# Kernel optimization log

Measured on AMD Instinct MI355X. Metric: run time of the kernel, lower is better.

The kernel has to match this reference:

```python
import jax, jax.numpy as jnp
import numpy as np

N = 50000      # nodes
E = 800000     # edges (avg degree 16)
F_IN = 512
HID = 128
OUT = 40


def setup_inputs() -> dict:
    key = jax.random.key(0)
    ks = jax.random.split(key, 6)
    x = jax.random.normal(ks[0], (N, F_IN), dtype=jnp.float32)
    edge_index = jax.random.randint(ks[1], (2, E), 0, N, dtype=jnp.int64)
    edge_weight = jax.random.uniform(ks[2], (E,), dtype=jnp.float32)
    # Glorot-ish init for the two GCNConv weight matrices
    W1 = jax.random.normal(ks[3], (F_IN, HID), dtype=jnp.float32) * (1.0 / np.sqrt(F_IN))
    b1 = jnp.zeros((HID,), dtype=jnp.float32)
    W2 = jax.random.normal(ks[4], (HID, OUT), dtype=jnp.float32) * (1.0 / np.sqrt(HID))
    b2 = jnp.zeros((OUT,), dtype=jnp.float32)
    return {"x": x, "edge_index": edge_index, "edge_weight": edge_weight,
            "W1": W1, "b1": b1, "W2": W2, "b2": b2}


def gcn_layer(x, edge_index, edge_weight, W, b):
    """PyG GCNConv (normalize=True, add_self_loops=True):
    out = D^{-1/2} (A + I) D^{-1/2} (x @ W) + b, with weighted edges."""
    n = x.shape[0]
    h = x @ W  # [n, F_out] dense transform before aggregation
    sl = jnp.arange(n)
    row = jnp.concatenate([edge_index[0], sl])   # source nodes
    col = jnp.concatenate([edge_index[1], sl])   # target nodes
    w = jnp.concatenate([edge_weight, jnp.ones((n,), x.dtype)])  # self-loop weight 1
    deg = jax.ops.segment_sum(w, col, num_segments=n)            # in-degree (weighted)
    dinv = jnp.where(deg > 0, jax.lax.rsqrt(deg), 0.0)
    norm = dinv[row] * w * dinv[col]                             # per-edge coefficient
    # gather-source, scale, scatter-add into target
    out = jax.ops.segment_sum(h[row] * norm[:, None], col, num_segments=n)
    return out + b


def reference(x, edge_index, edge_weight, W1, b1, W2, b2):
    h = jax.nn.relu(gcn_layer(x, edge_index, edge_weight, W1, b1))
    # dropout is identity at inference (training=False)
    h = gcn_layer(h, edge_index, edge_weight, W2, b2)
    return jax.nn.log_softmax(h, axis=1)
```

## Files before the change

kernel.cpp:

```cpp
#include <hip/hip_runtime.h>
#include <math.h>

#define N_NODES 50000
#define F_IN    512
#define HID     128
#define OUT_C   40
#define NPAD    48
#define E_EDGES 800000
#define SCAN_BLOCKS 196
#define LDA 40
#define LDK 136
#define MAXDEG 96
#define G1B 391
#define DEGB 3125

typedef __attribute__((ext_vector_type(8))) short short8;
typedef __attribute__((ext_vector_type(4))) float f32x4;

__device__ __forceinline__ unsigned short f2bf(float f) {
    union { float f; unsigned u; } v; v.f = f;
    unsigned u = v.u + 0x7fffu + ((v.u >> 16) & 1u);
    return (unsigned short)(u >> 16);
}
__device__ __forceinline__ float bf2f(unsigned short h) {
    return __uint_as_float((unsigned)h << 16);
}


__global__ void k_init(unsigned long long* __restrict__ packed) {
    int i = blockIdx.x * blockDim.x + threadIdx.x;
    if (i < N_NODES) packed[i] = 0ULL;
}


__global__ __launch_bounds__(256) void k_wprep(const float* __restrict__ W1,
                                               const float* __restrict__ W2,
                                               unsigned short* __restrict__ W1bt,
                                               unsigned short* __restrict__ W2bt) {
    int idx = blockIdx.x * 256 + threadIdx.x;
    if (idx < F_IN * HID) {
        int k = idx & 511, n = idx >> 9;
        W1bt[(size_t)n * F_IN + k] = f2bf(W1[(size_t)k * HID + n]);
    } else if (idx < F_IN * HID + NPAD * HID) {
        int i2 = idx - F_IN * HID;
        int k = i2 & 127, n = i2 >> 7;
        W2bt[n * HID + k] = (n < OUT_C) ? f2bf(W2[(size_t)k * OUT_C + n]) : 0;
    }
}


__global__ __launch_bounds__(256) void k_g1deg(const float* __restrict__ X,
                                               const unsigned short* __restrict__ W1bt,
                                               unsigned short* __restrict__ Hb,
                                               const int* __restrict__ col,
                                               const float* __restrict__ ew,
                                               unsigned long long* __restrict__ packed,
                                               int* __restrict__ rank) {
    const int tid = threadIdx.x;
    if (blockIdx.x >= G1B) {
        int e = (blockIdx.x - G1B) * 256 + tid;
        if (e < E_EDGES) {
            int c = col[e];
            unsigned long long fx = (unsigned long long)(ew[e] * 4294967296.0f);
            unsigned long long old = atomicAdd(&packed[c], (1ULL << 40) | fx);
            rank[e] = (int)(old >> 40);
        }
        return;
    }

    __shared__ __align__(16) unsigned short As[128 * LDA];
    __shared__ __align__(16) unsigned short Bs[128 * LDA];
    const int row0 = blockIdx.x * 128;
    const int lane = tid & 63;
    const int w    = tid >> 6;
    const int quad = lane >> 4;
    const int l16  = lane & 15;
    const int wm   = (w >> 1) * 64;
    const int wn   = (w & 1) * 64;

    f32x4 acc[4][4] = {};

    const int sr = tid >> 1;
    const int kg = (tid & 1) * 16;
    int arow = row0 + sr;
    if (arow >= N_NODES) arow = N_NODES - 1;
    const float*          xp = X + (size_t)arow * F_IN + kg;
    const unsigned short* bp = W1bt + (size_t)sr * F_IN + kg;
    unsigned short* asw = &As[sr * LDA + kg];
    unsigned short* bsw = &Bs[sr * LDA + kg];

    for (int k0 = 0; k0 < F_IN; k0 += 32) {
        float4 xa = *(const float4*)(xp + k0);
        float4 xb = *(const float4*)(xp + k0 + 4);
        float4 xc = *(const float4*)(xp + k0 + 8);
        float4 xd = *(const float4*)(xp + k0 + 12);
        short8 pa, pb;
        pa[0] = (short)f2bf(xa.x); pa[1] = (short)f2bf(xa.y);
        pa[2] = (short)f2bf(xa.z); pa[3] = (short)f2bf(xa.w);
        pa[4] = (short)f2bf(xb.x); pa[5] = (short)f2bf(xb.y);
        pa[6] = (short)f2bf(xb.z); pa[7] = (short)f2bf(xb.w);
        pb[0] = (short)f2bf(xc.x); pb[1] = (short)f2bf(xc.y);
        pb[2] = (short)f2bf(xc.z); pb[3] = (short)f2bf(xc.w);
        pb[4] = (short)f2bf(xd.x); pb[5] = (short)f2bf(xd.y);
        pb[6] = (short)f2bf(xd.z); pb[7] = (short)f2bf(xd.w);
        short8 wa = *(const short8*)(bp + k0);
        short8 wb = *(const short8*)(bp + k0 + 8);

        *(short8*)(asw)     = pa;
        *(short8*)(asw + 8) = pb;
        *(short8*)(bsw)     = wa;
        *(short8*)(bsw + 8) = wb;
        __syncthreads();

        short8 af[4], bf[4];
#pragma unroll
        for (int i = 0; i < 4; i++)
            af[i] = *(const short8*)&As[(wm + i * 16 + l16) * LDA + quad * 8];
#pragma unroll
        for (int j = 0; j < 4; j++)
            bf[j] = *(const short8*)&Bs[(wn + j * 16 + l16) * LDA + quad * 8];
#pragma unroll
        for (int i = 0; i < 4; i++)
#pragma unroll
            for (int j = 0; j < 4; j++)
                acc[i][j] = __builtin_amdgcn_mfma_f32_16x16x32_bf16(
                    af[i], bf[j], acc[i][j], 0, 0, 0);
        __syncthreads();
    }

#pragma unroll
    for (int i = 0; i < 4; i++) {
#pragma unroll
        for (int r = 0; r < 4; r++) {
            int grow = row0 + wm + i * 16 + quad * 4 + r;
            if (grow < N_NODES) {
#pragma unroll
                for (int j = 0; j < 4; j++) {
                    int gcol = wn + j * 16 + l16;
                    Hb[(size_t)grow * HID + gcol] = f2bf(acc[i][j][r]);
                }
            }
        }
    }
}


__global__ __launch_bounds__(256) void k_scan1(const unsigned long long* __restrict__ packed,
                                               int* __restrict__ excl,
                                               int* __restrict__ bsum,
                                               float* __restrict__ dinv) {
    __shared__ int s[256];
    int tid = threadIdx.x;
    int i = blockIdx.x * 256 + tid;
    unsigned long long pk = (i < N_NODES) ? packed[i] : 0ULL;
    int v = (int)(pk >> 40);
    if (i < N_NODES) {
        float d = 1.0f + (float)(pk & 0xFFFFFFFFFFULL) * (1.0f / 4294967296.0f);
        dinv[i] = rsqrtf(d);
    }
    s[tid] = v;
    __syncthreads();
#pragma unroll
    for (int off = 1; off < 256; off <<= 1) {
        int t = (tid >= off) ? s[tid - off] : 0;
        __syncthreads();
        s[tid] += t;
        __syncthreads();
    }
    if (i < N_NODES) excl[i] = s[tid] - v;
    if (tid == 255) bsum[blockIdx.x] = s[255];
}

__global__ __launch_bounds__(256) void k_scan2(int* __restrict__ bsum) {
    __shared__ int s[256];
    int tid = threadIdx.x;
    int v = (tid < SCAN_BLOCKS) ? bsum[tid] : 0;
    s[tid] = v;
    __syncthreads();
#pragma unroll
    for (int off = 1; off < 256; off <<= 1) {
        int t = (tid >= off) ? s[tid - off] : 0;
        __syncthreads();
        s[tid] += t;
        __syncthreads();
    }
    if (tid < SCAN_BLOCKS) bsum[tid] = s[tid] - v;
}

__global__ __launch_bounds__(256) void k_scan3(int* __restrict__ rowptr,
                                               const int* __restrict__ bsum) {
    int i = blockIdx.x * 256 + threadIdx.x;
    if (i < N_NODES) rowptr[i] += bsum[blockIdx.x];
    if (i == 0) rowptr[N_NODES] = E_EDGES;
}


__global__ void k_scatter(const int* __restrict__ row, const int* __restrict__ col,
                          const float* __restrict__ w, const float* __restrict__ dinv,
                          const int* __restrict__ rowptr, const int* __restrict__ rank,
                          int2* __restrict__ es) {
    int e = blockIdx.x * blockDim.x + threadIdx.x;
    if (e < E_EDGES) {
        int r = row[e], c = col[e];
        float pre = dinv[r] * w[e];
        int pos = rowptr[c] + rank[e];
        es[pos] = make_int2(r, __float_as_int(pre));
    }
}


__global__ __launch_bounds__(256) void k_agg1_csr(const int* __restrict__ rowptr,
                                                  const int2* __restrict__ es,
                                                  const float* __restrict__ dinv,
                                                  const unsigned short* __restrict__ H1b,
                                                  const float* __restrict__ b1,
                                                  unsigned short* __restrict__ A1b) {
    __shared__ int2 sE[4][MAXDEG];
    const int tid  = threadIdx.x;
    const int wv   = tid >> 6;
    const int lane = tid & 63;
    const int node = blockIdx.x * 4 + wv;
    if (node >= N_NODES) return;

    const int beg = rowptr[node];
    const int d   = rowptr[node + 1] - beg;
    const int dl  = (d < MAXDEG) ? d : MAXDEG;
    const int dp  = (dl + 7) & ~7;
    for (int p = lane; p < dp; p += 64)
        sE[wv][p] = (p < dl) ? es[beg + p] : make_int2(0, 0);

    const float di = dinv[node];
    const unsigned self = *(const unsigned*)&H1b[(size_t)node * HID + lane * 2];
    float al0 = di * __uint_as_float(self << 16);
    float ah0 = di * __uint_as_float(self & 0xffff0000u);
    float al1 = 0.0f, ah1 = 0.0f, al2 = 0.0f, ah2 = 0.0f, al3 = 0.0f, ah3 = 0.0f;

    for (int p = 0; p < dp; p += 8) {
        int s[8]; float n[8]; unsigned g[8];
#pragma unroll
        for (int j = 0; j < 8; j++) {
            int2 t = sE[wv][p + j];
            s[j] = t.x; n[j] = __int_as_float(t.y);
        }
#pragma unroll
        for (int j = 0; j < 8; j++)
            g[j] = *(const unsigned*)&H1b[(size_t)s[j] * HID + lane * 2];
        al0 = fmaf(__uint_as_float(g[0] << 16), n[0], al0);
        ah0 = fmaf(__uint_as_float(g[0] & 0xffff0000u), n[0], ah0);
        al1 = fmaf(__uint_as_float(g[1] << 16), n[1], al1);
        ah1 = fmaf(__uint_as_float(g[1] & 0xffff0000u), n[1], ah1);
        al2 = fmaf(__uint_as_float(g[2] << 16), n[2], al2);
        ah2 = fmaf(__uint_as_float(g[2] & 0xffff0000u), n[2], ah2);
        al3 = fmaf(__uint_as_float(g[3] << 16), n[3], al3);
        ah3 = fmaf(__uint_as_float(g[3] & 0xffff0000u), n[3], ah3);
        al0 = fmaf(__uint_as_float(g[4] << 16), n[4], al0);
        ah0 = fmaf(__uint_as_float(g[4] & 0xffff0000u), n[4], ah0);
        al1 = fmaf(__uint_as_float(g[5] << 16), n[5], al1);
        ah1 = fmaf(__uint_as_float(g[5] & 0xffff0000u), n[5], ah1);
        al2 = fmaf(__uint_as_float(g[6] << 16), n[6], al2);
        ah2 = fmaf(__uint_as_float(g[6] & 0xffff0000u), n[6], ah2);
        al3 = fmaf(__uint_as_float(g[7] << 16), n[7], al3);
        ah3 = fmaf(__uint_as_float(g[7] & 0xffff0000u), n[7], ah3);
    }
    for (int q = dl; q < d; ++q) {
        int2 t = es[beg + q];
        unsigned g = *(const unsigned*)&H1b[(size_t)t.x * HID + lane * 2];
        float nm = __int_as_float(t.y);
        al0 = fmaf(__uint_as_float(g << 16), nm, al0);
        ah0 = fmaf(__uint_as_float(g & 0xffff0000u), nm, ah0);
    }

    const float accl = (al0 + al1) + (al2 + al3);
    const float acch = (ah0 + ah1) + (ah2 + ah3);
    const int c = lane * 2;
    float rx = fmaxf(fmaf(di, accl, b1[c]), 0.0f);
    float ry = fmaxf(fmaf(di, acch, b1[c + 1]), 0.0f);
    unsigned pack = (unsigned)f2bf(rx) | ((unsigned)f2bf(ry) << 16);
    *(unsigned*)&A1b[(size_t)node * HID + c] = pack;
}


__global__ __launch_bounds__(256) void k_gemm2_mfma(const unsigned short* __restrict__ A1b,
                                                    const unsigned short* __restrict__ W2bt,
                                                    unsigned short* __restrict__ H2b) {
    __shared__ __align__(16) unsigned short As[128 * LDK];
    __shared__ __align__(16) unsigned short Bs[NPAD * LDK];
    const int tid  = threadIdx.x;
    const int row0 = blockIdx.x * 128;
    const int lane = tid & 63;
    const int w    = tid >> 6;
    const int quad = lane >> 4;
    const int l16  = lane & 15;

#pragma unroll
    for (int i = 0; i < 8; i++) {
        int id = tid + i * 256;
        int r = id >> 4, kc = (id & 15) * 8;
        int ar = row0 + r; if (ar >= N_NODES) ar = N_NODES - 1;
        *(short8*)&As[r * LDK + kc] = *(const short8*)&A1b[(size_t)ar * HID + kc];
    }
#pragma unroll
    for (int i = 0; i < 3; i++) {
        int id = tid + i * 256;
        int n = id >> 4, kc = (id & 15) * 8;
        *(short8*)&Bs[n * LDK + kc] = *(const short8*)&W2bt[n * HID + kc];
    }
    __syncthreads();

    f32x4 acc[2][3] = {};
    const int rbase = w * 32;
#pragma unroll
    for (int ks = 0; ks < 4; ks++) {
        const int k0 = ks * 32 + quad * 8;
        short8 af[2], bf[3];
#pragma unroll
        for (int i = 0; i < 2; i++)
            af[i] = *(const short8*)&As[(rbase + i * 16 + l16) * LDK + k0];
#pragma unroll
        for (int j = 0; j < 3; j++)
            bf[j] = *(const short8*)&Bs[(j * 16 + l16) * LDK + k0];
#pragma unroll
        for (int i = 0; i < 2; i++)
#pragma unroll
            for (int j = 0; j < 3; j++)
                acc[i][j] = __builtin_amdgcn_mfma_f32_16x16x32_bf16(
                    af[i], bf[j], acc[i][j], 0, 0, 0);
    }

#pragma unroll
    for (int i = 0; i < 2; i++) {
#pragma unroll
        for (int r = 0; r < 4; r++) {
            int grow = row0 + rbase + i * 16 + quad * 4 + r;
            if (grow < N_NODES) {
#pragma unroll
                for (int j = 0; j < 3; j++)
                    H2b[(size_t)grow * NPAD + j * 16 + l16] = f2bf(acc[i][j][r]);
            }
        }
    }
}


__global__ __launch_bounds__(256) void k_agg2_lsm(const int* __restrict__ rowptr,
                                                  const int2* __restrict__ es,
                                                  const float* __restrict__ dinv,
                                                  const unsigned short* __restrict__ H2b,
                                                  const float* __restrict__ b2,
                                                  float* __restrict__ out) {
    __shared__ int2 sE[4][MAXDEG];
    const int tid  = threadIdx.x;
    const int wv   = tid >> 6;
    const int lane = tid & 63;
    const int node = blockIdx.x * 4 + wv;
    if (node >= N_NODES) return;

    const int beg = rowptr[node];
    const int d   = rowptr[node + 1] - beg;
    const int dl = (d < MAXDEG) ? d : MAXDEG;
    const int dp = (dl + 7) & ~7;
    for (int p = lane; p < dp; p += 64)
        sE[wv][p] = (p < dl) ? es[beg + p] : make_int2(0, 0);

    float di = dinv[node];
    float a0 = 0.0f, a1 = 0.0f, a2 = 0.0f, a3 = 0.0f;
    if (lane < OUT_C) a0 = di * bf2f(H2b[(size_t)node * NPAD + lane]);

    for (int p = 0; p < dp; p += 8) {
        int s[8]; float n[8], v[8];
#pragma unroll
        for (int j = 0; j < 8; j++) {
            int2 t = sE[wv][p + j];
            s[j] = t.x; n[j] = __int_as_float(t.y);
        }
#pragma unroll
        for (int j = 0; j < 8; j++)
            v[j] = (lane < OUT_C) ? bf2f(H2b[(size_t)s[j] * NPAD + lane]) : 0.0f;
        a0 = fmaf(v[0], n[0], a0);  a1 = fmaf(v[1], n[1], a1);
        a2 = fmaf(v[2], n[2], a2);  a3 = fmaf(v[3], n[3], a3);
        a0 = fmaf(v[4], n[4], a0);  a1 = fmaf(v[5], n[5], a1);
        a2 = fmaf(v[6], n[6], a2);  a3 = fmaf(v[7], n[7], a3);
    }
    for (int q = dl; q < d; ++q)
        if (lane < OUT_C) {
            int2 t = es[beg + q];
            a0 = fmaf(bf2f(H2b[(size_t)t.x * NPAD + lane]), __int_as_float(t.y), a0);
        }

    float acc = (a0 + a1) + (a2 + a3);
    float v = (lane < OUT_C) ? fmaf(di, acc, b2[lane]) : -INFINITY;

    float m = v;
#pragma unroll
    for (int off = 32; off > 0; off >>= 1) m = fmaxf(m, __shfl_xor(m, off));
    float ex = (lane < OUT_C) ? __expf(v - m) : 0.0f;
    float s = ex;
#pragma unroll
    for (int off = 32; off > 0; off >>= 1) s += __shfl_xor(s, off);
    if (lane < OUT_C) out[(size_t)node * OUT_C + lane] = v - m - __logf(s);
}


extern "C" void kernel_launch(void* const* d_in, const int* in_sizes, int n_in,
                              void* d_out, int out_size, void* d_ws, size_t ws_size,
                              hipStream_t stream) {
    const float* x  = (const float*)d_in[0];
    const int*   ei = (const int*)d_in[1];
    const float* ew = (const float*)d_in[2];
    const float* W1 = (const float*)d_in[3];
    const float* b1 = (const float*)d_in[4];
    const float* W2 = (const float*)d_in[5];
    const float* b2 = (const float*)d_in[6];
    float* out = (float*)d_out;

    const int* row = ei;
    const int* col = ei + E_EDGES;

    float* ws = (float*)d_ws;
    unsigned long long* packed = (unsigned long long*)ws;
    float* dinv   = ws + 100000;
    int*   rowptr = (int*)(ws + 150000);
    int*   bsum   = (int*)(ws + 200016);
    int2*  es     = (int2*)(ws + 200272);
    int*   rank   = (int*)(ws + 1800272);
    unsigned short* H1b  = (unsigned short*)(ws + 2600272);
    unsigned short* A1b  = (unsigned short*)(ws + 5800272);
    unsigned short* W1bt = (unsigned short*)(ws + 9000272);
    unsigned short* W2bt = (unsigned short*)(ws + 9033040);
    unsigned short* H2b  = (unsigned short*)(ws + 9036112);

    const int B = 256;

    k_init<<<(N_NODES + B - 1) / B, B, 0, stream>>>(packed);
    k_wprep<<<(F_IN * HID + NPAD * HID + B - 1) / B, B, 0, stream>>>(W1, W2, W1bt, W2bt);

    k_g1deg<<<G1B + DEGB, B, 0, stream>>>(x, W1bt, H1b, col, ew, packed, rank);

    k_scan1<<<SCAN_BLOCKS, B, 0, stream>>>(packed, rowptr, bsum, dinv);
    k_scan2<<<1, B, 0, stream>>>(bsum);
    k_scan3<<<SCAN_BLOCKS, B, 0, stream>>>(rowptr, bsum);

    k_scatter<<<(E_EDGES + B - 1) / B, B, 0, stream>>>(row, col, ew, dinv,
                                                       rowptr, rank, es);

    k_agg1_csr<<<(N_NODES + 3) / 4, B, 0, stream>>>(rowptr, es, dinv, H1b, b1, A1b);

    k_gemm2_mfma<<<(N_NODES + 127) / 128, B, 0, stream>>>(A1b, W2bt, H2b);

    k_agg2_lsm<<<(N_NODES + 3) / 4, B, 0, stream>>>(rowptr, es, dinv, H2b, b2, out);
}
```

Before: 309.0 us.

## Fuse init kernels, drop scan3, prefetch GEMM loads, split-wave edge aggregation

Merges the packed-counter init into the weight-prep kernel and removes the rowptr fix-up scan pass, so consumers compute row offsets as excl plus the block sum. The first GEMM now prefetches the next K-tile into registers during the current MMA step and swaps __syncthreads for raw barriers. Both aggregation kernels split each wavefront into two halves that handle alternate 8-edge groups with wider per-lane loads, then combine the halves with a shuffle. Layer 2 has each lane handle two output channels, and log-softmax reduces over 32 lanes. This removes launches and raises memory-level parallelism, but adds extra index arithmetic and more register use.

```diff
diff --git a/kernel.cpp b/kernel.cpp
--- a/kernel.cpp
+++ b/kernel.cpp
@@ -25,19 +25,17 @@
 __device__ __forceinline__ float bf2f(unsigned short h) {
     return __uint_as_float((unsigned)h << 16);
 }
-
-
-__global__ void k_init(unsigned long long* __restrict__ packed) {
-    int i = blockIdx.x * blockDim.x + threadIdx.x;
-    if (i < N_NODES) packed[i] = 0ULL;
-}
-
-
-__global__ __launch_bounds__(256) void k_wprep(const float* __restrict__ W1,
-                                               const float* __restrict__ W2,
-                                               unsigned short* __restrict__ W1bt,
-                                               unsigned short* __restrict__ W2bt) {
+__device__ __forceinline__ float bflo(unsigned u) { return __uint_as_float(u << 16); }
+__device__ __forceinline__ float bfhi(unsigned u) { return __uint_as_float(u & 0xffff0000u); }
+
+
+__global__ __launch_bounds__(256) void k_initwprep(const float* __restrict__ W1,
+                                                   const float* __restrict__ W2,
+                                                   unsigned short* __restrict__ W1bt,
+                                                   unsigned short* __restrict__ W2bt,
+                                                   unsigned long long* __restrict__ packed) {
     int idx = blockIdx.x * 256 + threadIdx.x;
+    if (idx < N_NODES) packed[idx] = 0ULL;
     if (idx < F_IN * HID) {
         int k = idx & 511, n = idx >> 9;
         W1bt[(size_t)n * F_IN + k] = f2bf(W1[(size_t)k * HID + n]);
@@ -89,11 +87,14 @@
     unsigned short* asw = &As[sr * LDA + kg];
     unsigned short* bsw = &Bs[sr * LDA + kg];
 
+    float4 xa = *(const float4*)(xp);
+    float4 xb = *(const float4*)(xp + 4);
+    float4 xc = *(const float4*)(xp + 8);
+    float4 xd = *(const float4*)(xp + 12);
+    short8 wa = *(const short8*)(bp);
+    short8 wb = *(const short8*)(bp + 8);
+
     for (int k0 = 0; k0 < F_IN; k0 += 32) {
-        float4 xa = *(const float4*)(xp + k0);
-        float4 xb = *(const float4*)(xp + k0 + 4);
-        float4 xc = *(const float4*)(xp + k0 + 8);
-        float4 xd = *(const float4*)(xp + k0 + 12);
         short8 pa, pb;
         pa[0] = (short)f2bf(xa.x); pa[1] = (short)f2bf(xa.y);
         pa[2] = (short)f2bf(xa.z); pa[3] = (short)f2bf(xa.w);
@@ -103,14 +104,24 @@
         pb[2] = (short)f2bf(xc.z); pb[3] = (short)f2bf(xc.w);
         pb[4] = (short)f2bf(xd.x); pb[5] = (short)f2bf(xd.y);
         pb[6] = (short)f2bf(xd.z); pb[7] = (short)f2bf(xd.w);
-        short8 wa = *(const short8*)(bp + k0);
-        short8 wb = *(const short8*)(bp + k0 + 8);
+        short8 cwa = wa, cwb = wb;
+
+        if (k0 + 32 < F_IN) {
+            xa = *(const float4*)(xp + k0 + 32);
+            xb = *(const float4*)(xp + k0 + 36);
+            xc = *(const float4*)(xp + k0 + 40);
+            xd = *(const float4*)(xp + k0 + 44);
+            wa = *(const short8*)(bp + k0 + 32);
+            wb = *(const short8*)(bp + k0 + 40);
+        }
 
         *(short8*)(asw)     = pa;
         *(short8*)(asw + 8) = pb;
-        *(short8*)(bsw)     = wa;
-        *(short8*)(bsw + 8) = wb;
-        __syncthreads();
+        *(short8*)(bsw)     = cwa;
+        *(short8*)(bsw + 8) = cwb;
+        asm volatile("s_waitcnt lgkmcnt(0)" ::: "memory");
+        __builtin_amdgcn_s_barrier();
+        asm volatile("" ::: "memory");
 
         short8 af[4], bf[4];
 #pragma unroll
@@ -125,7 +136,9 @@
             for (int j = 0; j < 4; j++)
                 acc[i][j] = __builtin_amdgcn_mfma_f32_16x16x32_bf16(
                     af[i], bf[j], acc[i][j], 0, 0, 0);
-        __syncthreads();
+        asm volatile("" ::: "memory");
+        __builtin_amdgcn_s_barrier();
+        asm volatile("" ::: "memory");
     }
 
 #pragma unroll
@@ -187,29 +200,24 @@
     if (tid < SCAN_BLOCKS) bsum[tid] = s[tid] - v;
 }
 
-__global__ __launch_bounds__(256) void k_scan3(int* __restrict__ rowptr,
-                                               const int* __restrict__ bsum) {
-    int i = blockIdx.x * 256 + threadIdx.x;
-    if (i < N_NODES) rowptr[i] += bsum[blockIdx.x];
-    if (i == 0) rowptr[N_NODES] = E_EDGES;
-}
-
 
 __global__ void k_scatter(const int* __restrict__ row, const int* __restrict__ col,
                           const float* __restrict__ w, const float* __restrict__ dinv,
-                          const int* __restrict__ rowptr, const int* __restrict__ rank,
+                          const int* __restrict__ excl, const int* __restrict__ bsum,
+                          const int* __restrict__ rank,
                           int2* __restrict__ es) {
     int e = blockIdx.x * blockDim.x + threadIdx.x;
     if (e < E_EDGES) {
         int r = row[e], c = col[e];
         float pre = dinv[r] * w[e];
-        int pos = rowptr[c] + rank[e];
+        int pos = excl[c] + bsum[c >> 8] + rank[e];
         es[pos] = make_int2(r, __float_as_int(pre));
     }
 }
 
 
-__global__ __launch_bounds__(256) void k_agg1_csr(const int* __restrict__ rowptr,
+__global__ __launch_bounds__(256) void k_agg1_csr(const int* __restrict__ excl,
+                                                  const int* __restrict__ bsum,
                                                   const int2* __restrict__ es,
                                                   const float* __restrict__ dinv,
                                                   const unsigned short* __restrict__ H1b,
@@ -221,62 +229,74 @@
     const int lane = tid & 63;
     const int node = blockIdx.x * 4 + wv;
     if (node >= N_NODES) return;
-
-    const int beg = rowptr[node];
-    const int d   = rowptr[node + 1] - beg;
-    const int dl  = (d < MAXDEG) ? d : MAXDEG;
-    const int dp  = (dl + 7) & ~7;
+    const int h = lane >> 5;
+    const int l = lane & 31;
+
+    const int beg = excl[node] + bsum[node >> 8];
+    const int end = (node == N_NODES - 1) ? E_EDGES
+                                          : excl[node + 1] + bsum[(node + 1) >> 8];
+    const int d  = end - beg;
+    const int dl = (d < MAXDEG) ? d : MAXDEG;
+    const int dp = (dl + 15) & ~15;
     for (int p = lane; p < dp; p += 64)
         sE[wv][p] = (p < dl) ? es[beg + p] : make_int2(0, 0);
 
     const float di = dinv[node];
-    const unsigned self = *(const unsigned*)&H1b[(size_t)node * HID + lane * 2];
-    float al0 = di * __uint_as_float(self << 16);
-    float ah0 = di * __uint_as_float(self & 0xffff0000u);
-    float al1 = 0.0f, ah1 = 0.0f, al2 = 0.0f, ah2 = 0.0f, al3 = 0.0f, ah3 = 0.0f;
-
-    for (int p = 0; p < dp; p += 8) {
-        int s[8]; float n[8]; unsigned g[8];
+    const uint2 sv = *(const uint2*)&H1b[(size_t)node * HID + l * 4];
+    float a0, a1, a2, a3;
+    if (h == 0) {
+        a0 = di * bflo(sv.x); a1 = di * bfhi(sv.x);
+        a2 = di * bflo(sv.y); a3 = di * bfhi(sv.y);
+    } else {
+        a0 = a1 = a2 = a3 = 0.0f;
+    }
+
+    for (int p = 0; p < dp; p += 16) {
+        const int base = p + h * 8;
+        int s_[8]; float n_[8];
 #pragma unroll
         for (int j = 0; j < 8; j++) {
-            int2 t = sE[wv][p + j];
-            s[j] = t.x; n[j] = __int_as_float(t.y);
-        }
+            int2 t = sE[wv][base + j];
+            s_[j] = t.x; n_[j] = __int_as_float(t.y);
+        }
+        uint2 g[8];
 #pragma unroll
         for (int j = 0; j < 8; j++)
-            g[j] = *(const unsigned*)&H1b[(size_t)s[j] * HID + lane * 2];
-        al0 = fmaf(__uint_as_float(g[0] << 16), n[0], al0);
-        ah0 = fmaf(__uint_as_float(g[0] & 0xffff0000u), n[0], ah0);
-        al1 = fmaf(__uint_as_float(g[1] << 16), n[1], al1);
-        ah1 = fmaf(__uint_as_float(g[1] & 0xffff0000u), n[1], ah1);
-        al2 = fmaf(__uint_as_float(g[2] << 16), n[2], al2);
-        ah2 = fmaf(__uint_as_float(g[2] & 0xffff0000u), n[2], ah2);
-        al3 = fmaf(__uint_as_float(g[3] << 16), n[3], al3);
-        ah3 = fmaf(__uint_as_float(g[3] & 0xffff0000u), n[3], ah3);
-        al0 = fmaf(__uint_as_float(g[4] << 16), n[4], al0);
-        ah0 = fmaf(__uint_as_float(g[4] & 0xffff0000u), n[4], ah0);
-        al1 = fmaf(__uint_as_float(g[5] << 16), n[5], al1);
-        ah1 = fmaf(__uint_as_float(g[5] & 0xffff0000u), n[5], ah1);
-        al2 = fmaf(__uint_as_float(g[6] << 16), n[6], al2);
-        ah2 = fmaf(__uint_as_float(g[6] & 0xffff0000u), n[6], ah2);
-        al3 = fmaf(__uint_as_float(g[7] << 16), n[7], al3);
-        ah3 = fmaf(__uint_as_float(g[7] & 0xffff0000u), n[7], ah3);
-    }
-    for (int q = dl; q < d; ++q) {
+            g[j] = *(const uint2*)&H1b[(size_t)s_[j] * HID + l * 4];
+#pragma unroll
+        for (int j = 0; j < 8; j++) {
+            a0 = fmaf(bflo(g[j].x), n_[j], a0);
+            a1 = fmaf(bfhi(g[j].x), n_[j], a1);
+            a2 = fmaf(bflo(g[j].y), n_[j], a2);
+            a3 = fmaf(bfhi(g[j].y), n_[j], a3);
+        }
+    }
+    for (int q = dl + h; q < d; q += 2) {
         int2 t = es[beg + q];
-        unsigned g = *(const unsigned*)&H1b[(size_t)t.x * HID + lane * 2];
+        uint2 g = *(const uint2*)&H1b[(size_t)t.x * HID + l * 4];
         float nm = __int_as_float(t.y);
-        al0 = fmaf(__uint_as_float(g << 16), nm, al0);
-        ah0 = fmaf(__uint_as_float(g & 0xffff0000u), nm, ah0);
-    }
-
-    const float accl = (al0 + al1) + (al2 + al3);
-    const float acch = (ah0 + ah1) + (ah2 + ah3);
-    const int c = lane * 2;
-    float rx = fmaxf(fmaf(di, accl, b1[c]), 0.0f);
-    float ry = fmaxf(fmaf(di, acch, b1[c + 1]), 0.0f);
-    unsigned pack = (unsigned)f2bf(rx) | ((unsigned)f2bf(ry) << 16);
-    *(unsigned*)&A1b[(size_t)node * HID + c] = pack;
+        a0 = fmaf(bflo(g.x), nm, a0);
+        a1 = fmaf(bfhi(g.x), nm, a1);
+        a2 = fmaf(bflo(g.y), nm, a2);
+        a3 = fmaf(bfhi(g.y), nm, a3);
+    }
+
+    a0 += __shfl_xor(a0, 32);
+    a1 += __shfl_xor(a1, 32);
+    a2 += __shfl_xor(a2, 32);
+    a3 += __shfl_xor(a3, 32);
+
+    if (h == 0) {
+        const float4 bv = *(const float4*)&b1[l * 4];
+        float r0 = fmaxf(fmaf(di, a0, bv.x), 0.0f);
+        float r1 = fmaxf(fmaf(di, a1, bv.y), 0.0f);
+        float r2 = fmaxf(fmaf(di, a2, bv.z), 0.0f);
+        float r3 = fmaxf(fmaf(di, a3, bv.w), 0.0f);
+        uint2 pk;
+        pk.x = (unsigned)f2bf(r0) | ((unsigned)f2bf(r1) << 16);
+        pk.y = (unsigned)f2bf(r2) | ((unsigned)f2bf(r3) << 16);
+        *(uint2*)&A1b[(size_t)node * HID + l * 4] = pk;
+    }
 }
 
 
@@ -342,7 +362,8 @@
 }
 
 
-__global__ __launch_bounds__(256) void k_agg2_lsm(const int* __restrict__ rowptr,
+__global__ __launch_bounds__(256) void k_agg2_lsm(const int* __restrict__ excl,
+                                                  const int* __restrict__ bsum,
                                                   const int2* __restrict__ es,
                                                   const float* __restrict__ dinv,
                                                   const unsigned short* __restrict__ H2b,
@@ -354,50 +375,77 @@
     const int lane = tid & 63;
     const int node = blockIdx.x * 4 + wv;
     if (node >= N_NODES) return;
-
-    const int beg = rowptr[node];
-    const int d   = rowptr[node + 1] - beg;
+    const int h = lane >> 5;
+    const int l = lane & 31;
+    const bool act = (l < 20);
+
+    const int beg = excl[node] + bsum[node >> 8];
+    const int end = (node == N_NODES - 1) ? E_EDGES
+                                          : excl[node + 1] + bsum[(node + 1) >> 8];
+    const int d  = end - beg;
     const int dl = (d < MAXDEG) ? d : MAXDEG;
-    const int dp = (dl + 7) & ~7;
+    const int dp = (dl + 15) & ~15;
     for (int p = lane; p < dp; p += 64)
         sE[wv][p] = (p < dl) ? es[beg + p] : make_int2(0, 0);
 
-    float di = dinv[node];
-    float a0 = 0.0f, a1 = 0.0f, a2 = 0.0f, a3 = 0.0f;
-    if (lane < OUT_C) a0 = di * bf2f(H2b[(size_t)node * NPAD + lane]);
-
-    for (int p = 0; p < dp; p += 8) {
-        int s[8]; float n[8], v[8];
+    const float di = dinv[node];
+    float a0 = 0.0f, a1 = 0.0f;
+    if (h == 0 && act) {
+        unsigned sv = *(const unsigned*)&H2b[(size_t)node * NPAD + 2 * l];
+        a0 = di * bflo(sv); a1 = di * bfhi(sv);
+    }
+
+    for (int p = 0; p < dp; p += 16) {
+        const int base = p + h * 8;
+        int s_[8]; float n_[8];
 #pragma unroll
         for (int j = 0; j < 8; j++) {
-            int2 t = sE[wv][p + j];
-            s[j] = t.x; n[j] = __int_as_float(t.y);
-        }
-#pragma unroll
-        for (int j = 0; j < 8; j++)
-            v[j] = (lane < OUT_C) ? bf2f(H2b[(size_t)s[j] * NPAD + lane]) : 0.0f;
-        a0 = fmaf(v[0], n[0], a0);  a1 = fmaf(v[1], n[1], a1);
-        a2 = fmaf(v[2], n[2], a2);  a3 = fmaf(v[3], n[3], a3);
-        a0 = fmaf(v[4], n[4], a0);  a1 = fmaf(v[5], n[5], a1);
-        a2 = fmaf(v[6], n[6], a2);  a3 = fmaf(v[7], n[7], a3);
-    }
-    for (int q = dl; q < d; ++q)
-        if (lane < OUT_C) {
+            int2 t = sE[wv][base + j];
+            s_[j] = t.x; n_[j] = __int_as_float(t.y);
+        }
+        if (act) {
+            unsigned g[8];
+#pragma unroll
+            for (int j = 0; j < 8; j++)
+                g[j] = *(const unsigned*)&H2b[(size_t)s_[j] * NPAD + 2 * l];
+#pragma unroll
+            for (int j = 0; j < 8; j++) {
+                a0 = fmaf(bflo(g[j]), n_[j], a0);
+                a1 = fmaf(bfhi(g[j]), n_[j], a1);
+            }
+        }
+    }
+    for (int q = dl + h; q < d; q += 2)
+        if (act) {
             int2 t = es[beg + q];
-            a0 = fmaf(bf2f(H2b[(size_t)t.x * NPAD + lane]), __int_as_float(t.y), a0);
-        }
-
-    float acc = (a0 + a1) + (a2 + a3);
-    float v = (lane < OUT_C) ? fmaf(di, acc, b2[lane]) : -INFINITY;
-
-    float m = v;
-#pragma unroll
-    for (int off = 32; off > 0; off >>= 1) m = fmaxf(m, __shfl_xor(m, off));
-    float ex = (lane < OUT_C) ? __expf(v - m) : 0.0f;
+            unsigned g = *(const unsigned*)&H2b[(size_t)t.x * NPAD + 2 * l];
+            float nm = __int_as_float(t.y);
+            a0 = fmaf(bflo(g), nm, a0);
+            a1 = fmaf(bfhi(g), nm, a1);
+        }
+
+    a0 += __shfl_xor(a0, 32);
+    a1 += __shfl_xor(a1, 32);
+
+    float v0 = 0.0f, v1 = 0.0f;
+    if (act) {
+        float2 bv = *(const float2*)&b2[2 * l];
+        v0 = fmaf(di, a0, bv.x);
+        v1 = fmaf(di, a1, bv.y);
+    }
+
+    float m = act ? fmaxf(v0, v1) : -INFINITY;
+#pragma unroll
+    for (int off = 16; off > 0; off >>= 1) m = fmaxf(m, __shfl_xor(m, off));
+    float ex = act ? (__expf(v0 - m) + __expf(v1 - m)) : 0.0f;
     float s = ex;
 #pragma unroll
-    for (int off = 32; off > 0; off >>= 1) s += __shfl_xor(s, off);
-    if (lane < OUT_C) out[(size_t)node * OUT_C + lane] = v - m - __logf(s);
+    for (int off = 16; off > 0; off >>= 1) s += __shfl_xor(s, off);
+    if (h == 0 && act) {
+        float lg = __logf(s);
+        *(float2*)&out[(size_t)node * OUT_C + 2 * l] =
+            make_float2(v0 - m - lg, v1 - m - lg);
+    }
 }
 
 
@@ -419,7 +467,7 @@
     float* ws = (float*)d_ws;
     unsigned long long* packed = (unsigned long long*)ws;
     float* dinv   = ws + 100000;
-    int*   rowptr = (int*)(ws + 150000);
+    int*   excl   = (int*)(ws + 150000);
     int*   bsum   = (int*)(ws + 200016);
     int2*  es     = (int2*)(ws + 200272);
     int*   rank   = (int*)(ws + 1800272);
@@ -431,21 +479,20 @@
 
     const int B = 256;
 
-    k_init<<<(N_NODES + B - 1) / B, B, 0, stream>>>(packed);
-    k_wprep<<<(F_IN * HID + NPAD * HID + B - 1) / B, B, 0, stream>>>(W1, W2, W1bt, W2bt);
+    k_initwprep<<<(F_IN * HID + NPAD * HID + B - 1) / B, B, 0, stream>>>(
+        W1, W2, W1bt, W2bt, packed);
 
     k_g1deg<<<G1B + DEGB, B, 0, stream>>>(x, W1bt, H1b, col, ew, packed, rank);
 
-    k_scan1<<<SCAN_BLOCKS, B, 0, stream>>>(packed, rowptr, bsum, dinv);
+    k_scan1<<<SCAN_BLOCKS, B, 0, stream>>>(packed, excl, bsum, dinv);
     k_scan2<<<1, B, 0, stream>>>(bsum);
-    k_scan3<<<SCAN_BLOCKS, B, 0, stream>>>(rowptr, bsum);
 
     k_scatter<<<(E_EDGES + B - 1) / B, B, 0, stream>>>(row, col, ew, dinv,
-                                                       rowptr, rank, es);
-
-    k_agg1_csr<<<(N_NODES + 3) / 4, B, 0, stream>>>(rowptr, es, dinv, H1b, b1, A1b);
+                                                       excl, bsum, rank, es);
+
+    k_agg1_csr<<<(N_NODES + 3) / 4, B, 0, stream>>>(excl, bsum, es, dinv, H1b, b1, A1b);
 
     k_gemm2_mfma<<<(N_NODES + 127) / 128, B, 0, stream>>>(A1b, W2bt, H2b);
 
-    k_agg2_lsm<<<(N_NODES + 3) / 4, B, 0, stream>>>(rowptr, es, dinv, H2b, b2, out);
-}
+    k_agg2_lsm<<<(N_NODES + 3) / 4, B, 0, stream>>>(excl, bsum, es, dinv, H2b, b2, out);
+}
```

New measurement: 273.3 us. 1.13x faster.
